# Performance work log

Hardware: AMD Instinct MI355X
Metric: run time of the kernel (lower is better)

The kernel has to match this reference:

```python
import jax, jax.numpy as jnp
import numpy as np

S = 2048
HIDDEN = 4096
NH, NKV, HD = 32, 8, 128
QPK = NH // NKV  # 4
BLOCK, LOCAL, VERT = 64, 16, 8
ROPE_BASE = 1.0e6
SCALE = 1.0 / HD  # mup scaling: head_dim / mup_attn_multiplier(=1.0)


def setup_inputs() -> dict:
    key = jax.random.key(0)
    ks = jax.random.split(key, 5)
    qkv_out = NKV * (QPK + 2) * HD  # 6144, head-major layout
    return {
        "positions": jnp.arange(S, dtype=jnp.int32),
        "hidden_states": jax.random.normal(ks[0], (S, HIDDEN), jnp.float32),
        "w_qkv": jax.random.normal(ks[1], (qkv_out, HIDDEN), jnp.float32) * 0.02,
        "b_qkv": jax.random.normal(ks[2], (qkv_out,), jnp.float32) * 0.02,
        "w_dense": jax.random.normal(ks[3], (HIDDEN, HIDDEN), jnp.float32) * 0.02,
        "b_dense": jax.random.normal(ks[4], (HIDDEN,), jnp.float32) * 0.02,
    }


def _rope(x, cos, sin):
    # NeoX-style (non-interleaved) rotary over full head_dim.
    # x: [S, n_heads, HD]; cos/sin: [S, HD//2]
    d2 = x.shape[-1] // 2
    x1, x2 = x[..., :d2], x[..., d2:]
    c, s = cos[:, None, :], sin[:, None, :]
    return jnp.concatenate([x1 * c - x2 * s, x2 * c + x1 * s], axis=-1)


def _blocksparse_mask(positions):
    # vllm phi3small pattern: block (qb,kb) active iff causal AND
    # (qb-kb < local_blocks OR (kb + head + 1) % vert_stride == 0), hetero heads.
    qb = positions // BLOCK                       # [S]
    heads = jnp.arange(NH, dtype=positions.dtype)
    diff = qb[:, None] - qb[None, :]              # [S,S]
    local = diff < LOCAL                          # [S,S]
    vert = ((qb[None, None, :] + heads[:, None, None] + 1) % VERT) == 0  # [NH,1,S]
    causal = positions[:, None] >= positions[None, :]                     # [S,S]
    return (local[None] | vert) & causal[None]    # [NH,S,S]


def reference(positions, hidden_states, w_qkv, b_qkv, w_dense, b_dense):
    seq = hidden_states.shape[0]
    qkv = hidden_states @ w_qkv.T + b_qkv                   # [S, 6144]
    qkv = qkv.reshape(seq, NKV, QPK + 2, HD)                # head-major split
    q = qkv[:, :, :QPK].reshape(seq, NH, HD)
    k = qkv[:, :, QPK]                                      # [S, NKV, HD]
    v = qkv[:, :, QPK + 1]

    pos = positions.astype(jnp.float32)  # rope_position_scale = 1.0
    inv_freq = 1.0 / (ROPE_BASE ** (jnp.arange(0, HD, 2, dtype=jnp.float32) / HD))
    freqs = pos[:, None] * inv_freq                          # [S, HD/2]
    cos, sin = jnp.cos(freqs), jnp.sin(freqs)
    q = _rope(q, cos, sin)
    k = _rope(k, cos, sin)

    # GQA: each kv head serves QPK query heads
    kx = jnp.repeat(k, QPK, axis=1)                          # [S, NH, HD]
    vx = jnp.repeat(v, QPK, axis=1)

    scores = jnp.einsum('qhd,khd->hqk', q, kx) * SCALE       # [NH,S,S]
    mask = _blocksparse_mask(positions)
    scores = jnp.where(mask, scores, -jnp.inf)  # diag always in local block -> no empty rows
    p = jax.nn.softmax(scores, axis=-1)
    out = jnp.einsum('hqk,khd->qhd', p, vx).reshape(seq, NH * HD)
    return out @ w_dense.T + b_dense
```

## Files before the change

kernel.cpp:

```cpp
#include <hip/hip_runtime.h>

#define S_LEN   2048
#define HID     4096
#define NHEADS  32
#define NKVH    8
#define HDIM    128
#define NQKV    6144
#define ATT_SCALE (1.0f/128.0f)

typedef unsigned short u16;
typedef __attribute__((ext_vector_type(8))) __bf16 bf16x8;
typedef __attribute__((ext_vector_type(4))) float  f32x4;

__device__ __forceinline__ u16 f2bf(float f) {
    union { float f; unsigned u; } x; x.f = f;
    unsigned u = x.u;
    u += 0x7fffu + ((u >> 16) & 1u);
    return (u16)(u >> 16);
}
__device__ __forceinline__ float bf2f(u16 v) {
    union { unsigned u; float f; } x; x.u = ((unsigned)v) << 16; return x.f;
}

__global__ __launch_bounds__(256) void cvt_bf16_kernel(const float* __restrict__ in,
                                                       u16* __restrict__ out, int n4) {
    int stride = gridDim.x * blockDim.x;
    for (int i = blockIdx.x * blockDim.x + threadIdx.x; i < n4; i += stride) {
        float4 v = *(const float4*)(in + (size_t)i * 4);
        ushort4 o = make_ushort4(f2bf(v.x), f2bf(v.y), f2bf(v.z), f2bf(v.w));
        *(ushort4*)(out + (size_t)i * 4) = o;
    }
}

#define BM 128
#define BN 128
#define BK 32

template <bool OUT_BF16>
__global__ __launch_bounds__(256) void gemm_bt_kernel(
    const u16* __restrict__ A,
    const u16* __restrict__ B,
    const float* __restrict__ bias,
    void* __restrict__ Cout,
    int M, int N, int K)
{
    __shared__ u16 Alds[2][BM][BK];
    __shared__ u16 Blds[2][BN][BK];

    const int tid  = threadIdx.x;
    const int wid  = tid >> 6;
    const int lane = tid & 63;
    const int ln   = lane & 15;
    const int quad = lane >> 4;
    const int wm   = (wid >> 1) * 64;
    const int wn   = (wid & 1) * 64;
    const int tileM = blockIdx.y * BM;
    const int tileN = blockIdx.x * BN;

    const int srow = lane >> 2;
    const int scol = ((lane & 3) ^ ((srow >> 1) & 3)) * 8;

    f32x4 acc[4][4];
    #pragma unroll
    for (int i = 0; i < 4; i++)
        #pragma unroll
        for (int j = 0; j < 4; j++) {
            f32x4 z = {0.f, 0.f, 0.f, 0.f};
            acc[i][j] = z;
        }

    auto stage = [&](int k, int buf) {
        const int k0 = k * BK;
        #pragma unroll
        for (int p = 0; p < 2; p++) {
            int r = p * 64 + wid * 16;
            const u16* ga = A + (size_t)(tileM + r + srow) * K + k0 + scol;
            const u16* gb = B + (size_t)(tileN + r + srow) * K + k0 + scol;
            __builtin_amdgcn_global_load_lds(
                (const __attribute__((address_space(1))) void*)ga,
                (__attribute__((address_space(3))) void*)&Alds[buf][r][0], 16, 0, 0);
            __builtin_amdgcn_global_load_lds(
                (const __attribute__((address_space(1))) void*)gb,
                (__attribute__((address_space(3))) void*)&Blds[buf][r][0], 16, 0, 0);
        }
    };

    const int nIter = K / BK;
    stage(0, 0);

    const int pc = (quad ^ ((ln >> 1) & 3)) * 8;

    for (int k = 0; k < nIter; k++) {
        const int buf = k & 1;
        __syncthreads();
        if (k + 1 < nIter) stage(k + 1, buf ^ 1);

        bf16x8 af[4], bfr[4];
        #pragma unroll
        for (int i = 0; i < 4; i++)
            af[i] = *(const bf16x8*)(&Alds[buf][wm + i * 16 + ln][pc]);
        #pragma unroll
        for (int j = 0; j < 4; j++)
            bfr[j] = *(const bf16x8*)(&Blds[buf][wn + j * 16 + ln][pc]);
        #pragma unroll
        for (int i = 0; i < 4; i++)
            #pragma unroll
            for (int j = 0; j < 4; j++)
                acc[i][j] = __builtin_amdgcn_mfma_f32_16x16x32_bf16(af[i], bfr[j], acc[i][j], 0, 0, 0);
    }

    #pragma unroll
    for (int i = 0; i < 4; i++) {
        #pragma unroll
        for (int j = 0; j < 4; j++) {
            int n = tileN + wn + j * 16 + ln;
            float bv = bias[n];
            #pragma unroll
            for (int r = 0; r < 4; r++) {
                int m = tileM + wm + i * 16 + quad * 4 + r;
                float v = acc[i][j][r] + bv;
                if (OUT_BF16)
                    ((u16*)Cout)[(size_t)m * N + n] = f2bf(v);
                else
                    ((float*)Cout)[(size_t)m * N + n] = v;
            }
        }
    }
}

__global__ __launch_bounds__(128) void rope_split_kernel(
    const u16* __restrict__ qkv, const int* __restrict__ positions,
    u16* __restrict__ qb_o, u16* __restrict__ kb_o, u16* __restrict__ vb_o)
{
    const int d   = threadIdx.x;
    const int pos = blockIdx.x;
    const int hy  = blockIdx.y;
    const float p = (float)positions[pos];

    if (hy >= NHEADS + NKVH) {
        int kv = hy - NHEADS - NKVH;
        const u16* src = qkv + (size_t)pos * NQKV + (kv * 6 + 5) * HDIM;
        vb_o[((size_t)kv * S_LEN + pos) * HDIM + d] = src[d];
        return;
    }
    const u16* src;
    u16* dst;
    if (hy < NHEADS) {
        int kv = hy >> 2, qi = hy & 3;
        src = qkv + (size_t)pos * NQKV + (kv * 6 + qi) * HDIM;
        dst = qb_o + ((size_t)hy * S_LEN + pos) * HDIM;
    } else {
        int kv = hy - NHEADS;
        src = qkv + (size_t)pos * NQKV + (kv * 6 + 4) * HDIM;
        dst = kb_o + ((size_t)kv * S_LEN + pos) * HDIM;
    }
    int d2 = d & 63;
    float inv = expf(-(float)d2 * (13.815510557964274f / 64.0f));
    float fr = p * inv;
    float s, c;
    sincosf(fr, &s, &c);
    float x1 = bf2f(src[d2]);
    float x2 = bf2f(src[d2 + 64]);
    float o = (d < 64) ? (x1 * c - x2 * s) : (x2 * c + x1 * s);
    dst[d] = f2bf(o);
}

__global__ __launch_bounds__(256, 4) void attn_bs_kernel(
    const u16* __restrict__ Q,
    const u16* __restrict__ K,
    const u16* __restrict__ V,
    u16* __restrict__ O)
{
    __shared__ u16 Ks[64 * 128];
    __shared__ u16 Vt[128 * 64];
    __shared__ u16 Ps[4][16 * 64];

    const int qb = (int)gridDim.x - 1 - (int)blockIdx.x;
    const int h  = blockIdx.y;
    const int kv = h >> 2;
    const int tid  = threadIdx.x;
    const int w    = tid >> 6;
    const int lane = tid & 63;
    const int ln   = lane & 15;
    const int quad = lane >> 4;

    bf16x8 aq[4];
    {
        const u16* Qg = Q + ((size_t)h * S_LEN + qb * 64 + w * 16 + ln) * HDIM + quad * 8;
        #pragma unroll
        for (int ks = 0; ks < 4; ks++)
            aq[ks] = *(const bf16x8*)(Qg + ks * 32);
    }

    f32x4 oacc[8];
    #pragma unroll
    for (int n = 0; n < 8; n++) { f32x4 z = {0.f,0.f,0.f,0.f}; oacc[n] = z; }
    float mrow[4] = {-1e30f, -1e30f, -1e30f, -1e30f};
    float lrow[4] = {0.f, 0.f, 0.f, 0.f};

    for (int kb = 0; kb <= qb; kb++) {
        bool sel = (qb - kb < 16) || (((kb + h + 1) & 7) == 0);
        if (!sel) continue;

        __syncthreads();

        const u16* Kg = K + ((size_t)kv * S_LEN + kb * 64) * HDIM;
        const u16* Vg = V + ((size_t)kv * S_LEN + kb * 64) * HDIM;

        #pragma unroll
        for (int p = 0; p < 4; p++) {
            int r0  = w * 16 + p * 4;
            int row = r0 + (lane >> 4);
            const u16* src = Kg + (size_t)row * HDIM + (((lane & 15) ^ (row & 7)) << 3);
            __builtin_amdgcn_global_load_lds(
                (const __attribute__((address_space(1))) void*)src,
                (__attribute__((address_space(3))) void*)&Ks[r0 * 128], 16, 0, 0);
        }

        {
            int dbase = w * 32;
            #pragma unroll
            for (int p = 0; p < 4; p++) {
                int d0 = dbase + p * 8;
                uint4 vv = *(const uint4*)(Vg + (size_t)lane * HDIM + d0);
                const u16* pvv = (const u16*)&vv;
                #pragma unroll
                for (int jj = 0; jj < 8; jj++) {
                    int d = d0 + jj;
                    Vt[d * 64 + ((((lane >> 3)) ^ (d & 7)) << 3) + (lane & 7)] = pvv[jj];
                }
            }
        }
        __syncthreads();

        f32x4 sacc[4];
        #pragma unroll
        for (int jj = 0; jj < 4; jj++) { f32x4 z = {0.f,0.f,0.f,0.f}; sacc[jj] = z; }
        __builtin_amdgcn_s_setprio(1);
        #pragma unroll
        for (int ks = 0; ks < 4; ks++) {
            #pragma unroll
            for (int jj = 0; jj < 4; jj++) {
                bf16x8 bk = *(const bf16x8*)(
                    &Ks[(jj * 16 + ln) * 128 + (((ks * 4 + quad) ^ (ln & 7)) << 3)]);
                sacc[jj] = __builtin_amdgcn_mfma_f32_16x16x32_bf16(aq[ks], bk, sacc[jj], 0, 0, 0);
            }
        }
        __builtin_amdgcn_s_setprio(0);

        #pragma unroll
        for (int r = 0; r < 4; r++) {
            float pv[4];
            float mx = -1e30f;
            const int qrow = w * 16 + quad * 4 + r;
            #pragma unroll
            for (int jj = 0; jj < 4; jj++) {
                float s = sacc[jj][r] * ATT_SCALE;
                if (kb == qb && (jj * 16 + ln) > qrow) s = -1e30f;
                pv[jj] = s;
                mx = fmaxf(mx, s);
            }
            #pragma unroll
            for (int off = 1; off < 16; off <<= 1)
                mx = fmaxf(mx, __shfl_xor(mx, off, 64));
            float mnew  = fmaxf(mrow[r], mx);
            float alpha = __expf(mrow[r] - mnew);
            float sum = 0.f;
            #pragma unroll
            for (int jj = 0; jj < 4; jj++) {
                float pe = __expf(pv[jj] - mnew);
                pv[jj] = pe;
                sum += pe;
            }
            #pragma unroll
            for (int off = 1; off < 16; off <<= 1)
                sum += __shfl_xor(sum, off, 64);
            lrow[r] = lrow[r] * alpha + sum;
            mrow[r] = mnew;
            #pragma unroll
            for (int n = 0; n < 8; n++) oacc[n][r] *= alpha;
            const int prow = quad * 4 + r;
            #pragma unroll
            for (int jj = 0; jj < 4; jj++)
                Ps[w][prow * 64 + (((jj * 2 + (ln >> 3)) ^ (prow & 7)) << 3) + (ln & 7)]
                    = f2bf(pv[jj]);
        }

        __builtin_amdgcn_s_setprio(1);
        #pragma unroll
        for (int kk = 0; kk < 2; kk++) {
            bf16x8 ap = *(const bf16x8*)(
                &Ps[w][ln * 64 + (((kk * 4 + quad) ^ (ln & 7)) << 3)]);
            #pragma unroll
            for (int n = 0; n < 8; n++) {
                bf16x8 bv = *(const bf16x8*)(
                    &Vt[(n * 16 + ln) * 64 + (((kk * 4 + quad) ^ (ln & 7)) << 3)]);
                oacc[n] = __builtin_amdgcn_mfma_f32_16x16x32_bf16(ap, bv, oacc[n], 0, 0, 0);
            }
        }
        __builtin_amdgcn_s_setprio(0);
    }

    #pragma unroll
    for (int n = 0; n < 8; n++) {
        #pragma unroll
        for (int r = 0; r < 4; r++) {
            int row = w * 16 + quad * 4 + r;
            int pos = qb * 64 + row;
            float o = oacc[n][r] / lrow[r];
            O[(size_t)pos * (NHEADS * HDIM) + h * HDIM + n * 16 + ln] = f2bf(o);
        }
    }
}

extern "C" void kernel_launch(void* const* d_in, const int* in_sizes, int n_in,
                              void* d_out, int out_size, void* d_ws, size_t ws_size,
                              hipStream_t stream) {
    const int*   positions = (const int*)d_in[0];
    const float* hidden    = (const float*)d_in[1];
    const float* w_qkv     = (const float*)d_in[2];
    const float* b_qkv     = (const float*)d_in[3];
    const float* w_dense   = (const float*)d_in[4];
    const float* b_dense   = (const float*)d_in[5];
    float* out = (float*)d_out;

    char* ws = (char*)d_ws;
    u16* ws_h    = (u16*)(ws);
    u16* ws_wqkv = (u16*)(ws + 16777216);
    u16* ws_wd   = (u16*)(ws + 67108864);
    u16* ws_qkv  = (u16*)(ws + 100663296);
    u16* ws_q    = (u16*)(ws + 125829120);
    u16* ws_k    = (u16*)(ws + 142606336);
    u16* ws_v    = (u16*)(ws + 146800640);
    u16* ws_attn = (u16*)(ws + 150994944);

    cvt_bf16_kernel<<<1024, 256, 0, stream>>>(hidden,  ws_h,    (S_LEN * HID) / 4);
    cvt_bf16_kernel<<<2048, 256, 0, stream>>>(w_qkv,   ws_wqkv, (NQKV * HID) / 4);
    cvt_bf16_kernel<<<2048, 256, 0, stream>>>(w_dense, ws_wd,   (HID * HID) / 4);

    gemm_bt_kernel<true><<<dim3(NQKV / BN, S_LEN / BM), 256, 0, stream>>>(
        ws_h, ws_wqkv, b_qkv, ws_qkv, S_LEN, NQKV, HID);

    rope_split_kernel<<<dim3(S_LEN, NHEADS + 2 * NKVH), 128, 0, stream>>>(
        ws_qkv, positions, ws_q, ws_k, ws_v);

    attn_bs_kernel<<<dim3(S_LEN / 64, NHEADS), 256, 0, stream>>>(ws_q, ws_k, ws_v, ws_attn);

    gemm_bt_kernel<false><<<dim3(HID / BN, S_LEN / BM), 256, 0, stream>>>(
        ws_attn, ws_wd, b_dense, out, S_LEN, HID, HID);
}
```

Baseline: 565.6 us.

## Add 256x256 eight-wave pipelined GEMM with direct-to-LDS loads for QKV projection

Introduces a new GEMM kernel for the QKV projection with 256x256 tiles, 512 threads, global_load_lds direct-to-shared loads, XOR-swizzled LDS layout, and a ping-pong double buffer that interleaves half-tile loads with MFMA quadrants. The aim is to raise data reuse per tile and hide global-load latency behind matrix math. With 8x24 = 192 blocks on a 256-CU device, occupancy is uneven, and 128KB of LDS per block limits residency. The dense output GEMM keeps the old kernel.

```diff
diff --git a/kernel.cpp b/kernel.cpp
--- a/kernel.cpp
+++ b/kernel.cpp
@@ -128,6 +128,178 @@
     }
 }
 
+#define TBM 256
+#define TBN 256
+#define TBK 64
+
+#define GFENCE() asm volatile("" ::: "memory")
+#define GSBAR()  do { GFENCE(); __builtin_amdgcn_s_barrier(); GFENCE(); } while (0)
+
+template <bool OUT_BF16>
+__global__ __launch_bounds__(512, 2) void gemm_bt8_kernel(
+    const u16* __restrict__ A,
+    const u16* __restrict__ B,
+    const float* __restrict__ bias,
+    void* __restrict__ Cout,
+    int M, int N, int K)
+{
+    __shared__ u16 lds[65536];
+
+    const int tid  = threadIdx.x;
+    const int wid  = tid >> 6;
+    const int lane = tid & 63;
+    const int ln   = lane & 15;
+    const int quad = lane >> 4;
+    const int wr   = wid >> 2;
+    const int wc   = wid & 3;
+    const int tileM = blockIdx.y * TBM;
+    const int tileN = blockIdx.x * TBN;
+
+    f32x4 acc[2][2][4][2];
+    #pragma unroll
+    for (int a = 0; a < 2; a++)
+        #pragma unroll
+        for (int b = 0; b < 2; b++)
+            #pragma unroll
+            for (int m = 0; m < 4; m++)
+                #pragma unroll
+                for (int n = 0; n < 2; n++) {
+                    f32x4 z = {0.f, 0.f, 0.f, 0.f};
+                    acc[a][b][m][n] = z;
+                }
+
+    const int srho  = lane >> 3;
+    const int scol0 = (lane & 7) << 3;
+
+    auto stage_half = [&](const u16* Mp, int tbase, int h, int kk, int bb, int isB) {
+        const int ldsbase = isB * 32768 + (bb * 2 + h) * 8192;
+        #pragma unroll
+        for (int s = 0; s < 2; s++) {
+            const int rho0 = s * 64 + wid * 8;
+            const int rho  = rho0 + srho;
+            const int col  = scol0 ^ (((rho >> 2) & 1) << 4);
+            const u16* src = Mp + (size_t)(tbase + h * 128 + rho) * K + (size_t)kk * TBK + col;
+            __builtin_amdgcn_global_load_lds(
+                (const __attribute__((address_space(1))) void*)src,
+                (__attribute__((address_space(3))) void*)&lds[ldsbase + rho0 * 64], 16, 0, 0);
+        }
+    };
+
+    bf16x8 af[4][2];
+
+#define READ_A(a_)                                                                  \
+    do {                                                                            \
+        _Pragma("unroll")                                                           \
+        for (int m = 0; m < 4; m++) {                                               \
+            const int ra = wr * 64 + m * 16 + ln;                                   \
+            const int ab = (buf * 2 + (a_)) * 8192 + ra * 64;                       \
+            const int sw = ((ra >> 2) & 1) << 4;                                    \
+            af[m][0] = *(const bf16x8*)(&lds[ab + ((quad * 8) ^ sw)]);              \
+            af[m][1] = *(const bf16x8*)(&lds[ab + ((32 + quad * 8) ^ sw)]);         \
+        }                                                                           \
+    } while (0)
+
+#define READ_B(b_, bfr_)                                                            \
+    do {                                                                            \
+        _Pragma("unroll")                                                           \
+        for (int n = 0; n < 2; n++) {                                               \
+            const int rb = wc * 32 + n * 16 + ln;                                   \
+            const int bbase = 32768 + (buf * 2 + (b_)) * 8192 + rb * 64;            \
+            const int sw = ((rb >> 2) & 1) << 4;                                    \
+            bfr_[n][0] = *(const bf16x8*)(&lds[bbase + ((quad * 8) ^ sw)]);         \
+            bfr_[n][1] = *(const bf16x8*)(&lds[bbase + ((32 + quad * 8) ^ sw)]);    \
+        }                                                                           \
+    } while (0)
+
+#define DO_MFMA(a_, b_, bfr_)                                                       \
+    do {                                                                            \
+        __builtin_amdgcn_s_setprio(1);                                              \
+        _Pragma("unroll")                                                           \
+        for (int m = 0; m < 4; m++)                                                 \
+            _Pragma("unroll")                                                       \
+            for (int n = 0; n < 2; n++) {                                           \
+                acc[a_][b_][m][n] = __builtin_amdgcn_mfma_f32_16x16x32_bf16(        \
+                    af[m][0], bfr_[n][0], acc[a_][b_][m][n], 0, 0, 0);              \
+                acc[a_][b_][m][n] = __builtin_amdgcn_mfma_f32_16x16x32_bf16(        \
+                    af[m][1], bfr_[n][1], acc[a_][b_][m][n], 0, 0, 0);              \
+            }                                                                       \
+        __builtin_amdgcn_s_setprio(0);                                              \
+    } while (0)
+
+    const int nIter = K / TBK;
+
+    stage_half(A, tileM, 0, 0, 0, 0);
+    stage_half(B, tileN, 0, 0, 0, 1);
+    stage_half(A, tileM, 1, 0, 0, 0);
+    stage_half(B, tileN, 1, 0, 0, 1);
+
+    for (int t = 0; t < nIter; t++) {
+        const int buf = t & 1;
+        const int bn  = buf ^ 1;
+        const int kn  = (t + 1 == nIter) ? 0 : t + 1;
+
+        stage_half(A, tileM, 0, kn, bn, 0);
+        asm volatile("s_waitcnt vmcnt(6)" ::: "memory");
+        GSBAR();
+        {
+            bf16x8 bfr[2][2];
+            READ_A(0); READ_B(0, bfr);
+            DO_MFMA(0, 0, bfr);
+            GSBAR();
+
+            stage_half(B, tileN, 0, kn, bn, 1);
+            asm volatile("s_waitcnt vmcnt(4)" ::: "memory");
+            GSBAR();
+            READ_A(1);
+            DO_MFMA(1, 0, bfr);
+            GSBAR();
+        }
+
+        stage_half(A, tileM, 1, kn, bn, 0);
+        GSBAR();
+        {
+            bf16x8 bfr[2][2];
+            READ_B(1, bfr);
+            DO_MFMA(1, 1, bfr);
+            GSBAR();
+
+            stage_half(B, tileN, 1, kn, bn, 1);
+            GSBAR();
+            READ_A(0);
+            DO_MFMA(0, 1, bfr);
+            GSBAR();
+        }
+    }
+
+    asm volatile("s_waitcnt vmcnt(0)" ::: "memory");
+
+#undef READ_A
+#undef READ_B
+#undef DO_MFMA
+
+    #pragma unroll
+    for (int a = 0; a < 2; a++)
+        #pragma unroll
+        for (int b = 0; b < 2; b++)
+            #pragma unroll
+            for (int n = 0; n < 2; n++) {
+                #pragma unroll
+                for (int m = 0; m < 4; m++) {
+                    const int col = tileN + b * 128 + wc * 32 + n * 16 + ln;
+                    const float bv = bias[col];
+                    #pragma unroll
+                    for (int r = 0; r < 4; r++) {
+                        const int row = tileM + a * 128 + wr * 64 + m * 16 + quad * 4 + r;
+                        float v = acc[a][b][m][n][r] + bv;
+                        if (OUT_BF16)
+                            ((u16*)Cout)[(size_t)row * N + col] = f2bf(v);
+                        else
+                            ((float*)Cout)[(size_t)row * N + col] = v;
+                    }
+                }
+            }
+}
+
 __global__ __launch_bounds__(128) void rope_split_kernel(
     const u16* __restrict__ qkv, const int* __restrict__ positions,
     u16* __restrict__ qb_o, u16* __restrict__ kb_o, u16* __restrict__ vb_o)
@@ -338,7 +510,7 @@
     cvt_bf16_kernel<<<2048, 256, 0, stream>>>(w_qkv,   ws_wqkv, (NQKV * HID) / 4);
     cvt_bf16_kernel<<<2048, 256, 0, stream>>>(w_dense, ws_wd,   (HID * HID) / 4);
 
-    gemm_bt_kernel<true><<<dim3(NQKV / BN, S_LEN / BM), 256, 0, stream>>>(
+    gemm_bt8_kernel<true><<<dim3(NQKV / TBN, S_LEN / TBM), 512, 0, stream>>>(
         ws_h, ws_wqkv, b_qkv, ws_qkv, S_LEN, NQKV, HID);
 
     rope_split_kernel<<<dim3(S_LEN, NHEADS + 2 * NKVH), 128, 0, stream>>>(
```

New measurement: 575.9 us. About the same (+1.8%).

## Rewrite GEMMs with larger tiles, 8 waves and split-B staged pipeline

Applied to the files above, without the earlier changes.

Replaces the 128x128x32 GEMM with a 512-thread kernel using 128xBN tiles (384 for the QKV projection, 256 for the dense projection) and BK=64. B is staged in two halves, interleaved with MFMA work behind explicit vmcnt waits and raw barriers, with an XOR-swizzled LDS layout and setprio around MFMA bursts. The aim is higher arithmetic intensity per tile and better overlap of global-to-LDS loads with compute. In exchange, the grids are much smaller (256 blocks for the dense GEMM), and the hand-written waitcnt counts risk subtle hazards.

```diff
diff --git a/kernel.cpp b/kernel.cpp
--- a/kernel.cpp
+++ b/kernel.cpp
@@ -32,100 +32,163 @@
     }
 }
 
-#define BM 128
-#define BN 128
-#define BK 32
-
-template <bool OUT_BF16>
-__global__ __launch_bounds__(256) void gemm_bt_kernel(
+#define GFENCE() asm volatile("" ::: "memory")
+#define GSBAR()  do { GFENCE(); __builtin_amdgcn_s_barrier(); GFENCE(); } while (0)
+
+template <int BN_, int NB_, bool OUT_BF16>
+__global__ __launch_bounds__(512, 2) void gemm_fc_kernel(
     const u16* __restrict__ A,
     const u16* __restrict__ B,
     const float* __restrict__ bias,
     void* __restrict__ Cout,
     int M, int N, int K)
 {
-    __shared__ u16 Alds[2][BM][BK];
-    __shared__ u16 Blds[2][BN][BK];
+    constexpr int LB = BN_ / 128;
+    constexpr int VM = 2 + LB;
+    __shared__ u16 lds[16384 + 2 * BN_ * 64];
 
     const int tid  = threadIdx.x;
     const int wid  = tid >> 6;
     const int lane = tid & 63;
     const int ln   = lane & 15;
     const int quad = lane >> 4;
-    const int wm   = (wid >> 1) * 64;
-    const int wn   = (wid & 1) * 64;
-    const int tileM = blockIdx.y * BM;
-    const int tileN = blockIdx.x * BN;
-
-    const int srow = lane >> 2;
-    const int scol = ((lane & 3) ^ ((srow >> 1) & 3)) * 8;
-
-    f32x4 acc[4][4];
+    const int wr   = wid >> 2;
+    const int wc   = wid & 3;
+    const int tileM = blockIdx.y * 128;
+    const int tileN = blockIdx.x * BN_;
+
+    f32x4 acc[2][NB_][4];
     #pragma unroll
-    for (int i = 0; i < 4; i++)
-        #pragma unroll
-        for (int j = 0; j < 4; j++) {
-            f32x4 z = {0.f, 0.f, 0.f, 0.f};
-            acc[i][j] = z;
-        }
-
-    auto stage = [&](int k, int buf) {
-        const int k0 = k * BK;
-        #pragma unroll
-        for (int p = 0; p < 2; p++) {
-            int r = p * 64 + wid * 16;
-            const u16* ga = A + (size_t)(tileM + r + srow) * K + k0 + scol;
-            const u16* gb = B + (size_t)(tileN + r + srow) * K + k0 + scol;
-            __builtin_amdgcn_global_load_lds(
-                (const __attribute__((address_space(1))) void*)ga,
-                (__attribute__((address_space(3))) void*)&Alds[buf][r][0], 16, 0, 0);
-            __builtin_amdgcn_global_load_lds(
-                (const __attribute__((address_space(1))) void*)gb,
-                (__attribute__((address_space(3))) void*)&Blds[buf][r][0], 16, 0, 0);
-        }
+    for (int b = 0; b < 2; b++)
+        #pragma unroll
+        for (int n = 0; n < NB_; n++)
+            #pragma unroll
+            for (int m = 0; m < 4; m++) {
+                f32x4 z = {0.f, 0.f, 0.f, 0.f};
+                acc[b][n][m] = z;
+            }
+
+    const int srho = lane >> 3;
+    const int scol = (((lane & 7) ^ srho) << 3);
+
+    auto gload = [&](const u16* src, u16* dst) {
+        __builtin_amdgcn_global_load_lds(
+            (const __attribute__((address_space(1))) void*)src,
+            (__attribute__((address_space(3))) void*)dst, 16, 0, 0);
     };
-
-    const int nIter = K / BK;
-    stage(0, 0);
-
-    const int pc = (quad ^ ((ln >> 1) & 3)) * 8;
-
-    for (int k = 0; k < nIter; k++) {
-        const int buf = k & 1;
-        __syncthreads();
-        if (k + 1 < nIter) stage(k + 1, buf ^ 1);
-
-        bf16x8 af[4], bfr[4];
-        #pragma unroll
-        for (int i = 0; i < 4; i++)
-            af[i] = *(const bf16x8*)(&Alds[buf][wm + i * 16 + ln][pc]);
-        #pragma unroll
-        for (int j = 0; j < 4; j++)
-            bfr[j] = *(const bf16x8*)(&Blds[buf][wn + j * 16 + ln][pc]);
-        #pragma unroll
-        for (int i = 0; i < 4; i++)
-            #pragma unroll
-            for (int j = 0; j < 4; j++)
-                acc[i][j] = __builtin_amdgcn_mfma_f32_16x16x32_bf16(af[i], bfr[j], acc[i][j], 0, 0, 0);
-    }
+    auto stage_A = [&](int kk, int bb) {
+        const int base = bb * 8192;
+        #pragma unroll
+        for (int s = 0; s < 2; s++) {
+            const int rho0 = s * 64 + wid * 8;
+            const int rho  = rho0 + srho;
+            const u16* src = A + (size_t)(tileM + rho) * K + (size_t)kk * 64 + scol;
+            gload(src, &lds[base + rho0 * 64]);
+        }
+    };
+    auto stage_Bh = [&](int h, int kk, int bb) {
+        const int base = 16384 + bb * (BN_ * 64) + h * ((BN_ / 2) * 64);
+        #pragma unroll
+        for (int s = 0; s < LB; s++) {
+            const int rho0 = s * 64 + wid * 8;
+            const int rho  = rho0 + srho;
+            const u16* src = B + (size_t)(tileN + h * (BN_ / 2) + rho) * K
+                               + (size_t)kk * 64 + scol;
+            gload(src, &lds[base + rho0 * 64]);
+        }
+    };
+
+#define WAIT_VM()                                                                   \
+    do {                                                                            \
+        if constexpr (VM == 5) asm volatile("s_waitcnt vmcnt(5)" ::: "memory");     \
+        else                   asm volatile("s_waitcnt vmcnt(4)" ::: "memory");     \
+    } while (0)
+
+#define READ_A()                                                                    \
+    do {                                                                            \
+        _Pragma("unroll")                                                           \
+        for (int m = 0; m < 4; m++) {                                               \
+            const int ra = wr * 64 + m * 16 + ln;                                   \
+            const int ab = buf * 8192 + ra * 64;                                    \
+            const int rx = ra & 7;                                                  \
+            af[m][0] = *(const bf16x8*)(&lds[ab + ((quad ^ rx) << 3)]);             \
+            af[m][1] = *(const bf16x8*)(&lds[ab + (((4 + quad) ^ rx) << 3)]);       \
+        }                                                                           \
+    } while (0)
+
+#define MFMA_B(b_)                                                                  \
+    do {                                                                            \
+        __builtin_amdgcn_s_setprio(1);                                              \
+        _Pragma("unroll")                                                           \
+        for (int n = 0; n < NB_; n++) {                                             \
+            const int rb = (b_) * (BN_ / 2) + wc * (NB_ * 16) + n * 16 + ln;        \
+            const int bb = 16384 + buf * (BN_ * 64) + rb * 64;                      \
+            const int rx = rb & 7;                                                  \
+            bf16x8 b0 = *(const bf16x8*)(&lds[bb + ((quad ^ rx) << 3)]);            \
+            bf16x8 b1 = *(const bf16x8*)(&lds[bb + (((4 + quad) ^ rx) << 3)]);      \
+            _Pragma("unroll")                                                       \
+            for (int m = 0; m < 4; m++) {                                           \
+                acc[b_][n][m] = __builtin_amdgcn_mfma_f32_16x16x32_bf16(            \
+                    af[m][0], b0, acc[b_][n][m], 0, 0, 0);                          \
+                acc[b_][n][m] = __builtin_amdgcn_mfma_f32_16x16x32_bf16(            \
+                    af[m][1], b1, acc[b_][n][m], 0, 0, 0);                          \
+            }                                                                       \
+        }                                                                           \
+        __builtin_amdgcn_s_setprio(0);                                              \
+    } while (0)
+
+    const int nIter = K / 64;
+
+    stage_A(0, 0); stage_Bh(0, 0, 0); stage_Bh(1, 0, 0);
+
+    bf16x8 af[4][2];
+
+    for (int t = 0; t < nIter; t++) {
+        const int buf = t & 1;
+        const int bn  = buf ^ 1;
+        const int kn  = (t + 1 == nIter) ? 0 : t + 1;
+
+        stage_A(kn, bn);
+        WAIT_VM();
+        GSBAR();
+        READ_A();
+        MFMA_B(0);
+
+        stage_Bh(0, kn, bn);
+        WAIT_VM();
+        GSBAR();
+        MFMA_B(1);
+        stage_Bh(1, kn, bn);
+
+        asm volatile("s_waitcnt lgkmcnt(0)" ::: "memory");
+        GSBAR();
+    }
+
+    asm volatile("s_waitcnt vmcnt(0)" ::: "memory");
+
+#undef WAIT_VM
+#undef READ_A
+#undef MFMA_B
 
     #pragma unroll
-    for (int i = 0; i < 4; i++) {
-        #pragma unroll
-        for (int j = 0; j < 4; j++) {
-            int n = tileN + wn + j * 16 + ln;
-            float bv = bias[n];
-            #pragma unroll
-            for (int r = 0; r < 4; r++) {
-                int m = tileM + wm + i * 16 + quad * 4 + r;
-                float v = acc[i][j][r] + bv;
-                if (OUT_BF16)
-                    ((u16*)Cout)[(size_t)m * N + n] = f2bf(v);
-                else
-                    ((float*)Cout)[(size_t)m * N + n] = v;
-            }
-        }
-    }
+    for (int b = 0; b < 2; b++)
+        #pragma unroll
+        for (int n = 0; n < NB_; n++) {
+            const int col = tileN + b * (BN_ / 2) + wc * (NB_ * 16) + n * 16 + ln;
+            const float bv = bias[col];
+            #pragma unroll
+            for (int m = 0; m < 4; m++) {
+                #pragma unroll
+                for (int r = 0; r < 4; r++) {
+                    const int row = tileM + wr * 64 + m * 16 + quad * 4 + r;
+                    float v = acc[b][n][m][r] + bv;
+                    if (OUT_BF16)
+                        ((u16*)Cout)[(size_t)row * N + col] = f2bf(v);
+                    else
+                        ((float*)Cout)[(size_t)row * N + col] = v;
+                }
+            }
+        }
 }
 
 __global__ __launch_bounds__(128) void rope_split_kernel(
@@ -338,7 +401,7 @@
     cvt_bf16_kernel<<<2048, 256, 0, stream>>>(w_qkv,   ws_wqkv, (NQKV * HID) / 4);
     cvt_bf16_kernel<<<2048, 256, 0, stream>>>(w_dense, ws_wd,   (HID * HID) / 4);
 
-    gemm_bt_kernel<true><<<dim3(NQKV / BN, S_LEN / BM), 256, 0, stream>>>(
+    gemm_fc_kernel<384, 3, true><<<dim3(NQKV / 384, S_LEN / 128), 512, 0, stream>>>(
         ws_h, ws_wqkv, b_qkv, ws_qkv, S_LEN, NQKV, HID);
 
     rope_split_kernel<<<dim3(S_LEN, NHEADS + 2 * NKVH), 128, 0, stream>>>(
@@ -346,6 +409,6 @@
 
     attn_bs_kernel<<<dim3(S_LEN / 64, NHEADS), 256, 0, stream>>>(ws_q, ws_k, ws_v, ws_attn);
 
-    gemm_bt_kernel<false><<<dim3(HID / BN, S_LEN / BM), 256, 0, stream>>>(
+    gemm_fc_kernel<256, 2, false><<<dim3(HID / 256, S_LEN / 128), 512, 0, stream>>>(
         ws_attn, ws_wd, b_dense, out, S_LEN, HID, HID);
 }
```

Measured after the change: 520.9 us. 7.9% less time.
